# Optimization experiments

Measured on AMD Instinct MI355X. Metric: run time of the kernel, lower is better.

## Reference

```python
import jax, jax.numpy as jnp
import numpy as np

ALPHA = 0.1
THETA = 0.5
LAYERS = 4
N, E, D_IN, H, D_OUT = 100000, 1600000, 128, 128, 128


def setup_inputs() -> dict:
    key = jax.random.key(0)
    ks = jax.random.split(key, 9)
    x = jax.random.normal(ks[0], (N, D_IN), jnp.float32)
    edge_src = jax.random.randint(ks[1], (E,), 0, N, jnp.int32)
    edge_dst = jax.random.randint(ks[2], (E,), 0, N, jnp.int32)
    edge_w = jax.random.uniform(ks[3], (E,), jnp.float32)
    s_in = 1.0 / np.sqrt(D_IN)
    s_h = 1.0 / np.sqrt(H)
    W0 = jax.random.uniform(ks[4], (D_IN, H), jnp.float32, -s_in, s_in)
    b0 = jax.random.uniform(ks[5], (H,), jnp.float32, -s_in, s_in)
    W1 = jax.random.uniform(ks[6], (H, D_OUT), jnp.float32, -s_h, s_h)
    b1 = jax.random.uniform(ks[7], (D_OUT,), jnp.float32, -s_h, s_h)
    glorot = np.sqrt(6.0 / (H + H))
    convW = jax.random.uniform(ks[8], (LAYERS, H, H), jnp.float32, -glorot, glorot)
    return dict(x=x, edge_src=edge_src, edge_dst=edge_dst, edge_w=edge_w,
                W0=W0, b0=b0, W1=W1, b1=b1, convW=convW)


def reference(x, edge_src, edge_dst, edge_w, W0, b0, W1, b1, convW):
    # input projection + relu; x_0 is the initial residual (GCNII)
    h = jax.nn.relu(x @ W0 + b0)
    x0 = h
    for l in range(LAYERS):
        beta = float(np.log(THETA / (l + 1) + 1.0))
        # SpMM: agg[i] = sum_{(j->i) in E} w_e * h[j]
        msg = h[edge_src] * edge_w[:, None]                      # [E, H]
        agg = jax.ops.segment_sum(msg, edge_dst, num_segments=N)  # [N, H]
        out = (1.0 - ALPHA) * agg + ALPHA * x0                    # initial residual
        out = (1.0 - beta) * out + beta * (out @ convW[l])        # identity mapping
        h = jax.nn.relu(out)
    logits = h @ W1 + b1
    return jax.nn.log_softmax(logits, axis=-1)
```

## Files before the change

kernel.cpp:

```cpp
#include <hip/hip_runtime.h>
#include <math.h>

typedef unsigned int uint;
typedef unsigned short ushort;
using bf8   = __attribute__((ext_vector_type(8))) short;
using f32x4 = __attribute__((ext_vector_type(4))) float;

__device__ inline ushort f2bf(float f) {
  uint u = __float_as_uint(f);
  return (ushort)((u + 0x7fffu + ((u >> 16) & 1u)) >> 16);
}
__device__ inline float bf2f(ushort s) { return __uint_as_float(((uint)s) << 16); }
__device__ inline uint packbf2(float a, float b) {
  uint ua = __float_as_uint(a), ub = __float_as_uint(b);
  ua = (ua + 0x7fffu + ((ua >> 16) & 1u)) >> 16;
  ub = (ub + 0x7fffu + ((ub >> 16) & 1u)) & 0xffff0000u;
  return ua | ub;
}
__device__ inline float bflo(uint u) { return __uint_as_float(u << 16); }
__device__ inline float bfhi(uint u) { return __uint_as_float(u & 0xffff0000u); }

__global__ void hist_k(const int* __restrict__ dst, int* __restrict__ cnt, int E) {
  int tid = blockIdx.x * blockDim.x + threadIdx.x;
  int stride4 = gridDim.x * blockDim.x * 4;
  for (int base = tid * 4; base + 3 < E; base += stride4) {
    int4 d = *(const int4*)&dst[base];
    atomicAdd(&cnt[d.x], 1);
    atomicAdd(&cnt[d.y], 1);
    atomicAdd(&cnt[d.z], 1);
    atomicAdd(&cnt[d.w], 1);
  }
  int tail0 = (E & ~3);
  int e = tail0 + tid;
  if (e < E) atomicAdd(&cnt[dst[e]], 1);
}

__global__ __launch_bounds__(256) void scanA_k(const int* __restrict__ cnt,
                                               int* __restrict__ bsum, int N) {
  __shared__ int red[256];
  int tid = threadIdx.x;
  int i0 = blockIdx.x * 1024 + tid * 4;
  int s = 0;
  #pragma unroll
  for (int k = 0; k < 4; ++k) { int i = i0 + k; if (i < N) s += cnt[i]; }
  red[tid] = s;
  __syncthreads();
  for (int off = 128; off; off >>= 1) {
    if (tid < off) red[tid] += red[tid + off];
    __syncthreads();
  }
  if (tid == 0) bsum[blockIdx.x] = red[0];
}

__global__ __launch_bounds__(128) void scanB_k(const int* __restrict__ bsum,
                                               int* __restrict__ bbase, int nb) {
  __shared__ int buf[2][128];
  int tid = threadIdx.x;
  buf[0][tid] = (tid < nb) ? bsum[tid] : 0;
  __syncthreads();
  int pin = 0;
  for (int off = 1; off < 128; off <<= 1) {
    int x = buf[pin][tid];
    if (tid >= off) x += buf[pin][tid - off];
    buf[1 - pin][tid] = x;
    __syncthreads();
    pin = 1 - pin;
  }
  if (tid < nb) bbase[tid] = (tid == 0) ? 0 : buf[pin][tid - 1];
}

__global__ __launch_bounds__(256) void scanC_k(const int* __restrict__ cnt,
    const int* __restrict__ bbase, int* __restrict__ rp, int N, int E) {
  __shared__ int buf[2][256];
  int tid = threadIdx.x;
  int i0 = blockIdx.x * 1024 + tid * 4;
  int c[4]; int s = 0;
  #pragma unroll
  for (int k = 0; k < 4; ++k) { int i = i0 + k; c[k] = (i < N) ? cnt[i] : 0; s += c[k]; }
  buf[0][tid] = s;
  __syncthreads();
  int pin = 0;
  for (int off = 1; off < 256; off <<= 1) {
    int x = buf[pin][tid];
    if (tid >= off) x += buf[pin][tid - off];
    buf[1 - pin][tid] = x;
    __syncthreads();
    pin = 1 - pin;
  }
  int run = bbase[blockIdx.x] + buf[pin][tid] - s;
  #pragma unroll
  for (int k = 0; k < 4; ++k) {
    int i = i0 + k;
    if (i < N) { rp[i] = run; run += c[k]; }
  }
  if (blockIdx.x == 0 && tid == 0) rp[N] = E;
}

__global__ void scatter_k(const int* __restrict__ src, const int* __restrict__ dst,
                          const float* __restrict__ w, const int* __restrict__ rp,
                          int* __restrict__ cnt, int2* __restrict__ epk, int E) {
  int stride = gridDim.x * blockDim.x;
  for (int e = blockIdx.x * blockDim.x + threadIdx.x; e < E; e += stride) {
    int d = dst[e];
    int off = atomicAdd(&cnt[d], -1) - 1;
    epk[rp[d] + off] = make_int2(src[e], __float_as_int(w[e]));
  }
}

__global__ __launch_bounds__(256) void spmm_k(const int* __restrict__ rp,
    const int2* __restrict__ epk, const ushort* __restrict__ hbf,
    const ushort* __restrict__ x0bf, ushort* __restrict__ outbf, int N) {
  int node = (blockIdx.x * blockDim.x + threadIdx.x) >> 4;
  int l16 = threadIdx.x & 15;
  if (node >= N) return;
  int b = rp[node], e = rp[node + 1];
  float a0 = 0.f, a1 = 0.f, a2 = 0.f, a3 = 0.f;
  float a4 = 0.f, a5 = 0.f, a6 = 0.f, a7 = 0.f;
  const uint4* hb4 = (const uint4*)hbf;
  int j = b;
  for (; j + 3 < e; j += 4) {
    int2 e0 = epk[j], e1 = epk[j + 1], e2 = epk[j + 2], e3 = epk[j + 3];
    float w0 = __int_as_float(e0.y), w1 = __int_as_float(e1.y);
    float w2 = __int_as_float(e2.y), w3 = __int_as_float(e3.y);
    uint4 h0 = hb4[(size_t)e0.x * 16 + l16];
    uint4 h1 = hb4[(size_t)e1.x * 16 + l16];
    uint4 h2 = hb4[(size_t)e2.x * 16 + l16];
    uint4 h3 = hb4[(size_t)e3.x * 16 + l16];
    a0 = fmaf(w0, bflo(h0.x), a0); a1 = fmaf(w0, bfhi(h0.x), a1);
    a2 = fmaf(w0, bflo(h0.y), a2); a3 = fmaf(w0, bfhi(h0.y), a3);
    a4 = fmaf(w0, bflo(h0.z), a4); a5 = fmaf(w0, bfhi(h0.z), a5);
    a6 = fmaf(w0, bflo(h0.w), a6); a7 = fmaf(w0, bfhi(h0.w), a7);
    a0 = fmaf(w1, bflo(h1.x), a0); a1 = fmaf(w1, bfhi(h1.x), a1);
    a2 = fmaf(w1, bflo(h1.y), a2); a3 = fmaf(w1, bfhi(h1.y), a3);
    a4 = fmaf(w1, bflo(h1.z), a4); a5 = fmaf(w1, bfhi(h1.z), a5);
    a6 = fmaf(w1, bflo(h1.w), a6); a7 = fmaf(w1, bfhi(h1.w), a7);
    a0 = fmaf(w2, bflo(h2.x), a0); a1 = fmaf(w2, bfhi(h2.x), a1);
    a2 = fmaf(w2, bflo(h2.y), a2); a3 = fmaf(w2, bfhi(h2.y), a3);
    a4 = fmaf(w2, bflo(h2.z), a4); a5 = fmaf(w2, bfhi(h2.z), a5);
    a6 = fmaf(w2, bflo(h2.w), a6); a7 = fmaf(w2, bfhi(h2.w), a7);
    a0 = fmaf(w3, bflo(h3.x), a0); a1 = fmaf(w3, bfhi(h3.x), a1);
    a2 = fmaf(w3, bflo(h3.y), a2); a3 = fmaf(w3, bfhi(h3.y), a3);
    a4 = fmaf(w3, bflo(h3.z), a4); a5 = fmaf(w3, bfhi(h3.z), a5);
    a6 = fmaf(w3, bflo(h3.w), a6); a7 = fmaf(w3, bfhi(h3.w), a7);
  }
  for (; j < e; ++j) {
    int2 e0 = epk[j];
    float w0 = __int_as_float(e0.y);
    uint4 h0 = hb4[(size_t)e0.x * 16 + l16];
    a0 = fmaf(w0, bflo(h0.x), a0); a1 = fmaf(w0, bfhi(h0.x), a1);
    a2 = fmaf(w0, bflo(h0.y), a2); a3 = fmaf(w0, bfhi(h0.y), a3);
    a4 = fmaf(w0, bflo(h0.z), a4); a5 = fmaf(w0, bfhi(h0.z), a5);
    a6 = fmaf(w0, bflo(h0.w), a6); a7 = fmaf(w0, bfhi(h0.w), a7);
  }
  uint4 xv = ((const uint4*)x0bf)[(size_t)node * 16 + l16];
  float o0 = 0.9f * a0 + 0.1f * bflo(xv.x);
  float o1 = 0.9f * a1 + 0.1f * bfhi(xv.x);
  float o2 = 0.9f * a2 + 0.1f * bflo(xv.y);
  float o3 = 0.9f * a3 + 0.1f * bfhi(xv.y);
  float o4 = 0.9f * a4 + 0.1f * bflo(xv.z);
  float o5 = 0.9f * a5 + 0.1f * bfhi(xv.z);
  float o6 = 0.9f * a6 + 0.1f * bflo(xv.w);
  float o7 = 0.9f * a7 + 0.1f * bfhi(xv.w);
  uint4 u;
  u.x = packbf2(o0, o1); u.y = packbf2(o2, o3);
  u.z = packbf2(o4, o5); u.w = packbf2(o6, o7);
  ((uint4*)outbf)[(size_t)node * 16 + l16] = u;
}

template<int MODE, int ABF>
__global__ __launch_bounds__(256, 4) void gemm_mfma(const void* __restrict__ inv,
    const float* __restrict__ W, const float* __restrict__ bias,
    float* __restrict__ outf, ushort* __restrict__ outbf, ushort* __restrict__ outbf2,
    float cin, float cw, int N) {
  __shared__ ushort Wt[128][136];
  const float*  inf = (const float*)inv;
  const ushort* inb = (const ushort*)inv;
  int tid = threadIdx.x;

  for (int i = tid; i < 128 * 32; i += 256) {
    int k = i >> 5, n4 = (i & 31) << 2;
    float4 v = *(const float4*)&W[(size_t)k * 128 + n4];
    Wt[n4 + 0][k] = f2bf(v.x);
    Wt[n4 + 1][k] = f2bf(v.y);
    Wt[n4 + 2][k] = f2bf(v.z);
    Wt[n4 + 3][k] = f2bf(v.w);
  }
  __syncthreads();

  int w = tid >> 6, lane = tid & 63;
  int l15 = lane & 15, hi = lane >> 4;
  int rbase = blockIdx.x * 128 + w * 32;

  f32x4 acc[2][8];
  #pragma unroll
  for (int mi = 0; mi < 2; ++mi)
    #pragma unroll
    for (int ni = 0; ni < 8; ++ni)
      acc[mi][ni] = (f32x4){0.f, 0.f, 0.f, 0.f};

  int r0 = min(rbase + l15, N - 1);
  int r1 = min(rbase + 16 + l15, N - 1);

  #pragma unroll
  for (int kt = 0; kt < 4; ++kt) {
    int koff = kt * 32 + hi * 8;
    bf8 a0, a1;
    if (ABF) {
      a0 = *(const bf8*)&inb[(size_t)r0 * 128 + koff];
      a1 = *(const bf8*)&inb[(size_t)r1 * 128 + koff];
    } else {
      float4 f0 = *(const float4*)&inf[(size_t)r0 * 128 + koff];
      float4 f1 = *(const float4*)&inf[(size_t)r0 * 128 + koff + 4];
      float4 g0 = *(const float4*)&inf[(size_t)r1 * 128 + koff];
      float4 g1 = *(const float4*)&inf[(size_t)r1 * 128 + koff + 4];
      union { bf8 v; uint u[4]; } ta, tb;
      ta.u[0] = packbf2(f0.x, f0.y); ta.u[1] = packbf2(f0.z, f0.w);
      ta.u[2] = packbf2(f1.x, f1.y); ta.u[3] = packbf2(f1.z, f1.w);
      tb.u[0] = packbf2(g0.x, g0.y); tb.u[1] = packbf2(g0.z, g0.w);
      tb.u[2] = packbf2(g1.x, g1.y); tb.u[3] = packbf2(g1.z, g1.w);
      a0 = ta.v; a1 = tb.v;
    }
    #pragma unroll
    for (int ni = 0; ni < 8; ++ni) {
      bf8 b = *(const bf8*)&Wt[ni * 16 + l15][koff];
      acc[0][ni] = __builtin_amdgcn_mfma_f32_16x16x32_bf16(a0, b, acc[0][ni], 0, 0, 0);
      acc[1][ni] = __builtin_amdgcn_mfma_f32_16x16x32_bf16(a1, b, acc[1][ni], 0, 0, 0);
    }
  }

  float bcol[8];
  if (MODE != 1) {
    #pragma unroll
    for (int ni = 0; ni < 8; ++ni) bcol[ni] = bias[ni * 16 + l15];
  }

  #pragma unroll
  for (int mi = 0; mi < 2; ++mi) {
    #pragma unroll
    for (int reg = 0; reg < 4; ++reg) {
      int row = rbase + mi * 16 + 4 * hi + reg;
      bool valid = (row < N);
      float y[8];
      #pragma unroll
      for (int ni = 0; ni < 8; ++ni) y[ni] = acc[mi][ni][reg];
      if (MODE == 1) {
        if (valid) {
          #pragma unroll
          for (int ni = 0; ni < 8; ++ni) {
            float iv = bf2f(inb[(size_t)row * 128 + ni * 16 + l15]);
            y[ni] = fmaxf(cin * iv + cw * y[ni], 0.f);
          }
        }
      } else {
        #pragma unroll
        for (int ni = 0; ni < 8; ++ni) y[ni] += bcol[ni];
        if (MODE == 0) {
          #pragma unroll
          for (int ni = 0; ni < 8; ++ni) y[ni] = fmaxf(y[ni], 0.f);
        }
      }
      if (MODE == 2) {
        float m = y[0];
        #pragma unroll
        for (int ni = 1; ni < 8; ++ni) m = fmaxf(m, y[ni]);
        #pragma unroll
        for (int off = 1; off <= 8; off <<= 1) m = fmaxf(m, __shfl_xor(m, off));
        float s = 0.f;
        #pragma unroll
        for (int ni = 0; ni < 8; ++ni) s += expf(y[ni] - m);
        #pragma unroll
        for (int off = 1; off <= 8; off <<= 1) s += __shfl_xor(s, off);
        float lg = m + logf(s);
        #pragma unroll
        for (int ni = 0; ni < 8; ++ni) y[ni] -= lg;
      }
      if (valid) {
        if (MODE == 2) {
          #pragma unroll
          for (int ni = 0; ni < 8; ++ni)
            outf[(size_t)row * 128 + ni * 16 + l15] = y[ni];
        } else {
          #pragma unroll
          for (int ni = 0; ni < 8; ++ni) {
            ushort u = f2bf(y[ni]);
            outbf[(size_t)row * 128 + ni * 16 + l15] = u;
            if (MODE == 0) outbf2[(size_t)row * 128 + ni * 16 + l15] = u;
          }
        }
      }
    }
  }
}

extern "C" void kernel_launch(void* const* d_in, const int* in_sizes, int n_in,
                              void* d_out, int out_size, void* d_ws, size_t ws_size,
                              hipStream_t stream) {
  const float* x     = (const float*)d_in[0];
  const int*   esrc  = (const int*)d_in[1];
  const int*   edst  = (const int*)d_in[2];
  const float* ew    = (const float*)d_in[3];
  const float* W0    = (const float*)d_in[4];
  const float* b0    = (const float*)d_in[5];
  const float* W1    = (const float*)d_in[6];
  const float* b1    = (const float*)d_in[7];
  const float* convW = (const float*)d_in[8];
  int N = in_sizes[0] / 128;
  int E = in_sizes[1];
  float* outp = (float*)d_out;

  char* ws = (char*)d_ws;
  size_t off = 0;
  auto alloc = [&](size_t bytes) {
    void* p = ws + off;
    off += (bytes + 255) & ~(size_t)255;
    return p;
  };
  ushort* hbf   = (ushort*)alloc((size_t)N * 128 * 2);
  ushort* x0bf  = (ushort*)alloc((size_t)N * 128 * 2);
  ushort* bufB  = (ushort*)alloc((size_t)N * 128 * 2);
  ushort* bufA  = (ushort*)alloc((size_t)N * 128 * 2);
  int*    rp    = (int*)alloc((size_t)(N + 1) * 4);
  int*    cnt   = (int*)alloc((size_t)N * 4);
  int2*   epk   = (int2*)alloc((size_t)E * 8);
  int nbScan = (N + 1023) / 1024;
  int*    bsum  = (int*)alloc((size_t)nbScan * 4);
  int*    bbase = (int*)alloc((size_t)nbScan * 4);

  hipMemsetAsync(cnt, 0, (size_t)N * 4, stream);
  hist_k<<<2048, 256, 0, stream>>>(edst, cnt, E);
  scanA_k<<<nbScan, 256, 0, stream>>>(cnt, bsum, N);
  scanB_k<<<1, 128, 0, stream>>>(bsum, bbase, nbScan);
  scanC_k<<<nbScan, 256, 0, stream>>>(cnt, bbase, rp, N, E);
  scatter_k<<<2048, 256, 0, stream>>>(esrc, edst, ew, rp, cnt, epk, E);

  int gemmBlocks = (N + 127) / 128;
  int spmmBlocks = (N + 15) / 16;

  gemm_mfma<0, 0><<<gemmBlocks, 256, 0, stream>>>(x, W0, b0, nullptr, hbf, x0bf, 0.f, 1.f, N);

  for (int l = 0; l < 4; ++l) {
    float beta = logf(0.5f / (float)(l + 1) + 1.f);
    spmm_k<<<spmmBlocks, 256, 0, stream>>>(rp, epk, hbf, x0bf, bufB, N);
    gemm_mfma<1, 1><<<gemmBlocks, 256, 0, stream>>>(
        bufB, convW + (size_t)l * 128 * 128, nullptr,
        nullptr, (l == 3) ? bufA : hbf, nullptr,
        1.f - beta, beta, N);
  }

  gemm_mfma<2, 1><<<gemmBlocks, 256, 0, stream>>>(bufA, W1, b1, outp, nullptr, nullptr, 0.f, 1.f, N);
}
```

Baseline: 582.6 us.

## Store hidden features as fp8 and pack edges into 32-bit words

The hidden activations gathered by SpMM are now stored as unsigned fp8 (e4m3, non-negative after ReLU) instead of bf16. Edge records are packed into one 32-bit word holding a 17-bit source index and a 15-bit quantized weight. Together these halve the bytes moved in the dominant gather and the edge stream, and the SpMM loop is unrolled to 8 edges. Weight transposition to bf16 moves into a single prep kernel, so each GEMM block reads pre-transposed weights from global memory instead of rebuilding them in LDS. The cost is lower precision in activations and edge weights, and the 17-bit index field caps the node count.

```diff
diff --git a/kernel.cpp b/kernel.cpp
--- a/kernel.cpp
+++ b/kernel.cpp
@@ -3,8 +3,10 @@
 
 typedef unsigned int uint;
 typedef unsigned short ushort;
+typedef unsigned char uchar;
 using bf8   = __attribute__((ext_vector_type(8))) short;
 using f32x4 = __attribute__((ext_vector_type(4))) float;
+using f32x2 = __attribute__((ext_vector_type(2))) float;
 
 __device__ inline ushort f2bf(float f) {
   uint u = __float_as_uint(f);
@@ -19,6 +21,37 @@
 }
 __device__ inline float bflo(uint u) { return __uint_as_float(u << 16); }
 __device__ inline float bfhi(uint u) { return __uint_as_float(u & 0xffff0000u); }
+
+#if __has_builtin(__builtin_amdgcn_cvt_pk_f32_fp8)
+template<bool W>
+__device__ inline f32x2 fp8x2_f32(uint v) {
+  return __builtin_amdgcn_cvt_pk_f32_fp8((int)v, W);
+}
+#else
+__device__ inline float fp8_1(uint b) {
+  uint e = (b >> 3) & 15u, m = b & 7u;
+  float nrm = __uint_as_float(((e + 120u) << 23) | (m << 20));
+  float sub = (float)m * 0.001953125f;
+  return e ? nrm : sub;
+}
+template<bool W>
+__device__ inline f32x2 fp8x2_f32(uint v) {
+  uint sh = W ? 16u : 0u;
+  f32x2 r; r.x = fp8_1((v >> sh) & 0xffu); r.y = fp8_1((v >> (sh + 8)) & 0xffu);
+  return r;
+}
+#endif
+
+__device__ inline uint f32_fp8(float f) {
+  if (!(f > 0.f)) return 0u;
+  if (f >= 446.f) return 0x7eu;
+  if (f < 0.015625f) return (uint)(f * 512.f + 0.5f);
+  uint u = __float_as_uint(f);
+  uint r = u + 0x7ffffu + ((u >> 20) & 1u);
+  uint eb = r >> 23, mant = (r >> 20) & 7u;
+  if (eb > 135u || (eb == 135u && mant == 7u)) return 0x7eu;
+  return ((eb - 120u) << 3) | mant;
+}
 
 __global__ void hist_k(const int* __restrict__ dst, int* __restrict__ cnt, int E) {
   int tid = blockIdx.x * blockDim.x + threadIdx.x;
@@ -98,17 +131,36 @@
 
 __global__ void scatter_k(const int* __restrict__ src, const int* __restrict__ dst,
                           const float* __restrict__ w, const int* __restrict__ rp,
-                          int* __restrict__ cnt, int2* __restrict__ epk, int E) {
+                          int* __restrict__ cnt, uint* __restrict__ epk, int E) {
   int stride = gridDim.x * blockDim.x;
   for (int e = blockIdx.x * blockDim.x + threadIdx.x; e < E; e += stride) {
     int d = dst[e];
     int off = atomicAdd(&cnt[d], -1) - 1;
-    epk[rp[d] + off] = make_int2(src[e], __float_as_int(w[e]));
-  }
+    uint wq = (uint)(w[e] * 32767.f + 0.5f);
+    epk[rp[d] + off] = ((uint)src[e] << 15) | wq;
+  }
+}
+
+__global__ __launch_bounds__(256) void prepW_k(const float* __restrict__ W0,
+    const float* __restrict__ convW, const float* __restrict__ W1,
+    ushort* __restrict__ Wt) {
+  int b = blockIdx.x;
+  int m = b >> 4;
+  int n0 = (b & 15) * 8;
+  const float* W = (m == 0) ? W0 : (m <= 4) ? (convW + (size_t)(m - 1) * 128 * 128) : W1;
+  ushort* dst = Wt + (size_t)m * 128 * 128;
+  int t = threadIdx.x;
+  int n = n0 + (t >> 5);
+  int k0 = (t & 31) * 4;
+  float a = W[(size_t)(k0 + 0) * 128 + n];
+  float c = W[(size_t)(k0 + 1) * 128 + n];
+  float d = W[(size_t)(k0 + 2) * 128 + n];
+  float e = W[(size_t)(k0 + 3) * 128 + n];
+  *(uint2*)&dst[(size_t)n * 128 + k0] = make_uint2(packbf2(a, c), packbf2(d, e));
 }
 
 __global__ __launch_bounds__(256) void spmm_k(const int* __restrict__ rp,
-    const int2* __restrict__ epk, const ushort* __restrict__ hbf,
+    const uint* __restrict__ epk, const uchar* __restrict__ h8,
     const ushort* __restrict__ x0bf, ushort* __restrict__ outbf, int N) {
   int node = (blockIdx.x * blockDim.x + threadIdx.x) >> 4;
   int l16 = threadIdx.x & 15;
@@ -116,42 +168,45 @@
   int b = rp[node], e = rp[node + 1];
   float a0 = 0.f, a1 = 0.f, a2 = 0.f, a3 = 0.f;
   float a4 = 0.f, a5 = 0.f, a6 = 0.f, a7 = 0.f;
-  const uint4* hb4 = (const uint4*)hbf;
+  const uint2* hb = (const uint2*)h8;
+#define EDG(EU, HV) do { \
+    float wgt = (float)((EU) & 0x7fffu) * (1.f / 32767.f); \
+    f32x2 p0 = fp8x2_f32<false>((HV).x), p1 = fp8x2_f32<true>((HV).x); \
+    f32x2 p2 = fp8x2_f32<false>((HV).y), p3 = fp8x2_f32<true>((HV).y); \
+    a0 = fmaf(wgt, p0.x, a0); a1 = fmaf(wgt, p0.y, a1); \
+    a2 = fmaf(wgt, p1.x, a2); a3 = fmaf(wgt, p1.y, a3); \
+    a4 = fmaf(wgt, p2.x, a4); a5 = fmaf(wgt, p2.y, a5); \
+    a6 = fmaf(wgt, p3.x, a6); a7 = fmaf(wgt, p3.y, a7); \
+  } while (0)
   int j = b;
+  for (; j + 7 < e; j += 8) {
+    uint u0 = epk[j],     u1 = epk[j + 1], u2 = epk[j + 2], u3 = epk[j + 3];
+    uint u4 = epk[j + 4], u5 = epk[j + 5], u6 = epk[j + 6], u7 = epk[j + 7];
+    uint2 h0 = hb[(size_t)(u0 >> 15) * 16 + l16];
+    uint2 h1 = hb[(size_t)(u1 >> 15) * 16 + l16];
+    uint2 h2 = hb[(size_t)(u2 >> 15) * 16 + l16];
+    uint2 h3 = hb[(size_t)(u3 >> 15) * 16 + l16];
+    uint2 h4 = hb[(size_t)(u4 >> 15) * 16 + l16];
+    uint2 h5 = hb[(size_t)(u5 >> 15) * 16 + l16];
+    uint2 h6 = hb[(size_t)(u6 >> 15) * 16 + l16];
+    uint2 h7 = hb[(size_t)(u7 >> 15) * 16 + l16];
+    EDG(u0, h0); EDG(u1, h1); EDG(u2, h2); EDG(u3, h3);
+    EDG(u4, h4); EDG(u5, h5); EDG(u6, h6); EDG(u7, h7);
+  }
   for (; j + 3 < e; j += 4) {
-    int2 e0 = epk[j], e1 = epk[j + 1], e2 = epk[j + 2], e3 = epk[j + 3];
-    float w0 = __int_as_float(e0.y), w1 = __int_as_float(e1.y);
-    float w2 = __int_as_float(e2.y), w3 = __int_as_float(e3.y);
-    uint4 h0 = hb4[(size_t)e0.x * 16 + l16];
-    uint4 h1 = hb4[(size_t)e1.x * 16 + l16];
-    uint4 h2 = hb4[(size_t)e2.x * 16 + l16];
-    uint4 h3 = hb4[(size_t)e3.x * 16 + l16];
-    a0 = fmaf(w0, bflo(h0.x), a0); a1 = fmaf(w0, bfhi(h0.x), a1);
-    a2 = fmaf(w0, bflo(h0.y), a2); a3 = fmaf(w0, bfhi(h0.y), a3);
-    a4 = fmaf(w0, bflo(h0.z), a4); a5 = fmaf(w0, bfhi(h0.z), a5);
-    a6 = fmaf(w0, bflo(h0.w), a6); a7 = fmaf(w0, bfhi(h0.w), a7);
-    a0 = fmaf(w1, bflo(h1.x), a0); a1 = fmaf(w1, bfhi(h1.x), a1);
-    a2 = fmaf(w1, bflo(h1.y), a2); a3 = fmaf(w1, bfhi(h1.y), a3);
-    a4 = fmaf(w1, bflo(h1.z), a4); a5 = fmaf(w1, bfhi(h1.z), a5);
-    a6 = fmaf(w1, bflo(h1.w), a6); a7 = fmaf(w1, bfhi(h1.w), a7);
-    a0 = fmaf(w2, bflo(h2.x), a0); a1 = fmaf(w2, bfhi(h2.x), a1);
-    a2 = fmaf(w2, bflo(h2.y), a2); a3 = fmaf(w2, bfhi(h2.y), a3);
-    a4 = fmaf(w2, bflo(h2.z), a4); a5 = fmaf(w2, bfhi(h2.z), a5);
-    a6 = fmaf(w2, bflo(h2.w), a6); a7 = fmaf(w2, bfhi(h2.w), a7);
-    a0 = fmaf(w3, bflo(h3.x), a0); a1 = fmaf(w3, bfhi(h3.x), a1);
-    a2 = fmaf(w3, bflo(h3.y), a2); a3 = fmaf(w3, bfhi(h3.y), a3);
-    a4 = fmaf(w3, bflo(h3.z), a4); a5 = fmaf(w3, bfhi(h3.z), a5);
-    a6 = fmaf(w3, bflo(h3.w), a6); a7 = fmaf(w3, bfhi(h3.w), a7);
+    uint u0 = epk[j], u1 = epk[j + 1], u2 = epk[j + 2], u3 = epk[j + 3];
+    uint2 h0 = hb[(size_t)(u0 >> 15) * 16 + l16];
+    uint2 h1 = hb[(size_t)(u1 >> 15) * 16 + l16];
+    uint2 h2 = hb[(size_t)(u2 >> 15) * 16 + l16];
+    uint2 h3 = hb[(size_t)(u3 >> 15) * 16 + l16];
+    EDG(u0, h0); EDG(u1, h1); EDG(u2, h2); EDG(u3, h3);
   }
   for (; j < e; ++j) {
-    int2 e0 = epk[j];
-    float w0 = __int_as_float(e0.y);
-    uint4 h0 = hb4[(size_t)e0.x * 16 + l16];
-    a0 = fmaf(w0, bflo(h0.x), a0); a1 = fmaf(w0, bfhi(h0.x), a1);
-    a2 = fmaf(w0, bflo(h0.y), a2); a3 = fmaf(w0, bfhi(h0.y), a3);
-    a4 = fmaf(w0, bflo(h0.z), a4); a5 = fmaf(w0, bfhi(h0.z), a5);
-    a6 = fmaf(w0, bflo(h0.w), a6); a7 = fmaf(w0, bfhi(h0.w), a7);
-  }
+    uint u0 = epk[j];
+    uint2 h0 = hb[(size_t)(u0 >> 15) * 16 + l16];
+    EDG(u0, h0);
+  }
+#undef EDG
   uint4 xv = ((const uint4*)x0bf)[(size_t)node * 16 + l16];
   float o0 = 0.9f * a0 + 0.1f * bflo(xv.x);
   float o1 = 0.9f * a1 + 0.1f * bfhi(xv.x);
@@ -167,26 +222,14 @@
   ((uint4*)outbf)[(size_t)node * 16 + l16] = u;
 }
 
-template<int MODE, int ABF>
+template<int MODE, int ABF, int OUT8>
 __global__ __launch_bounds__(256, 4) void gemm_mfma(const void* __restrict__ inv,
-    const float* __restrict__ W, const float* __restrict__ bias,
+    const ushort* __restrict__ Wt, const float* __restrict__ bias,
     float* __restrict__ outf, ushort* __restrict__ outbf, ushort* __restrict__ outbf2,
-    float cin, float cw, int N) {
-  __shared__ ushort Wt[128][136];
+    uchar* __restrict__ out8, float cin, float cw, int N) {
   const float*  inf = (const float*)inv;
   const ushort* inb = (const ushort*)inv;
   int tid = threadIdx.x;
-
-  for (int i = tid; i < 128 * 32; i += 256) {
-    int k = i >> 5, n4 = (i & 31) << 2;
-    float4 v = *(const float4*)&W[(size_t)k * 128 + n4];
-    Wt[n4 + 0][k] = f2bf(v.x);
-    Wt[n4 + 1][k] = f2bf(v.y);
-    Wt[n4 + 2][k] = f2bf(v.z);
-    Wt[n4 + 3][k] = f2bf(v.w);
-  }
-  __syncthreads();
-
   int w = tid >> 6, lane = tid & 63;
   int l15 = lane & 15, hi = lane >> 4;
   int rbase = blockIdx.x * 128 + w * 32;
@@ -222,7 +265,7 @@
     }
     #pragma unroll
     for (int ni = 0; ni < 8; ++ni) {
-      bf8 b = *(const bf8*)&Wt[ni * 16 + l15][koff];
+      bf8 b = *(const bf8*)&Wt[(size_t)(ni * 16 + l15) * 128 + koff];
       acc[0][ni] = __builtin_amdgcn_mfma_f32_16x16x32_bf16(a0, b, acc[0][ni], 0, 0, 0);
       acc[1][ni] = __builtin_amdgcn_mfma_f32_16x16x32_bf16(a1, b, acc[1][ni], 0, 0, 0);
     }
@@ -282,9 +325,10 @@
         } else {
           #pragma unroll
           for (int ni = 0; ni < 8; ++ni) {
-            ushort u = f2bf(y[ni]);
-            outbf[(size_t)row * 128 + ni * 16 + l15] = u;
-            if (MODE == 0) outbf2[(size_t)row * 128 + ni * 16 + l15] = u;
+            size_t idx = (size_t)row * 128 + ni * 16 + l15;
+            if (OUT8) out8[idx] = (uchar)f32_fp8(y[ni]);
+            else      outbf[idx] = f2bf(y[ni]);
+            if (MODE == 0) outbf2[idx] = f2bf(y[ni]);
           }
         }
       }
@@ -315,19 +359,21 @@
     off += (bytes + 255) & ~(size_t)255;
     return p;
   };
-  ushort* hbf   = (ushort*)alloc((size_t)N * 128 * 2);
+  uchar*  h8    = (uchar*)alloc((size_t)N * 128);
   ushort* x0bf  = (ushort*)alloc((size_t)N * 128 * 2);
   ushort* bufB  = (ushort*)alloc((size_t)N * 128 * 2);
   ushort* bufA  = (ushort*)alloc((size_t)N * 128 * 2);
+  ushort* Wtg   = (ushort*)alloc((size_t)6 * 128 * 128 * 2);
   int*    rp    = (int*)alloc((size_t)(N + 1) * 4);
   int*    cnt   = (int*)alloc((size_t)N * 4);
-  int2*   epk   = (int2*)alloc((size_t)E * 8);
+  uint*   epk   = (uint*)alloc((size_t)E * 4);
   int nbScan = (N + 1023) / 1024;
   int*    bsum  = (int*)alloc((size_t)nbScan * 4);
   int*    bbase = (int*)alloc((size_t)nbScan * 4);
 
-  hipMemsetAsync(cnt, 0, (size_t)N * 4, stream);
+  (void)hipMemsetAsync(cnt, 0, (size_t)N * 4, stream);
   hist_k<<<2048, 256, 0, stream>>>(edst, cnt, E);
+  prepW_k<<<96, 256, 0, stream>>>(W0, convW, W1, Wtg);
   scanA_k<<<nbScan, 256, 0, stream>>>(cnt, bsum, N);
   scanB_k<<<1, 128, 0, stream>>>(bsum, bbase, nbScan);
   scanC_k<<<nbScan, 256, 0, stream>>>(cnt, bbase, rp, N, E);
@@ -336,16 +382,23 @@
   int gemmBlocks = (N + 127) / 128;
   int spmmBlocks = (N + 15) / 16;
 
-  gemm_mfma<0, 0><<<gemmBlocks, 256, 0, stream>>>(x, W0, b0, nullptr, hbf, x0bf, 0.f, 1.f, N);
+  gemm_mfma<0, 0, 1><<<gemmBlocks, 256, 0, stream>>>(
+      x, Wtg, b0, nullptr, nullptr, x0bf, h8, 0.f, 1.f, N);
 
   for (int l = 0; l < 4; ++l) {
     float beta = logf(0.5f / (float)(l + 1) + 1.f);
-    spmm_k<<<spmmBlocks, 256, 0, stream>>>(rp, epk, hbf, x0bf, bufB, N);
-    gemm_mfma<1, 1><<<gemmBlocks, 256, 0, stream>>>(
-        bufB, convW + (size_t)l * 128 * 128, nullptr,
-        nullptr, (l == 3) ? bufA : hbf, nullptr,
-        1.f - beta, beta, N);
-  }
-
-  gemm_mfma<2, 1><<<gemmBlocks, 256, 0, stream>>>(bufA, W1, b1, outp, nullptr, nullptr, 0.f, 1.f, N);
-}
+    spmm_k<<<spmmBlocks, 256, 0, stream>>>(rp, epk, h8, x0bf, bufB, N);
+    if (l < 3) {
+      gemm_mfma<1, 1, 1><<<gemmBlocks, 256, 0, stream>>>(
+          bufB, Wtg + (size_t)(1 + l) * 128 * 128, nullptr,
+          nullptr, nullptr, nullptr, h8, 1.f - beta, beta, N);
+    } else {
+      gemm_mfma<1, 1, 0><<<gemmBlocks, 256, 0, stream>>>(
+          bufB, Wtg + (size_t)(1 + l) * 128 * 128, nullptr,
+          nullptr, bufA, nullptr, nullptr, 1.f - beta, beta, N);
+    }
+  }
+
+  gemm_mfma<2, 1, 0><<<gemmBlocks, 256, 0, stream>>>(
+      bufA, Wtg + (size_t)5 * 128 * 128, b1, outp, nullptr, nullptr, nullptr, 0.f, 1.f, N);
+}
```

Measured after the change: 538.1 us. -7.6%, faster.
